# Optimization experiments

Hardware: AMD Instinct MI355X
Metric: run time of the kernel (lower is better)

## Reference

```python
import jax, jax.numpy as jnp
import numpy as np

T, B, P, F = 4096, 64, 512, 5
SHARP = 1.0
NEG_LARGE = -1e30


def setup_inputs() -> dict:
    key = jax.random.key(0)
    k1, k2, k3 = jax.random.split(key, 3)
    x = jax.random.normal(k1, (T, B, F), dtype=jnp.float32)
    # seqs index the 4 base features (feature 4 is the 'stay' score)
    seqs = jax.random.randint(k2, (B, P), 0, 4, dtype=jnp.int32)
    # seqlens index into fwd of width P+1, so valid range is [0, P]
    seqlens = jax.random.randint(k3, (B,), 0, P + 1, dtype=jnp.int32)
    return {"x": x, "seqs": seqs, "seqlens": seqlens}


def reference(x, seqs, seqlens):
    nt, nb, nf = x.shape
    ns = seqs.shape[1]
    # initial forward scores: -inf everywhere except position 0
    fwd0 = jnp.full((nb, ns + 1), NEG_LARGE, dtype=x.dtype).at[:, 0].set(0.0)
    xs = x * SHARP  # [T, B, F]

    def step(fwd, xt):
        # stay: emit the 'stay' feature (index 4), keep position
        stay = xt[:, 4][:, None] + fwd  # [B, P+1]
        # move: emit the base at each sequence position, advance by one
        move = jnp.take_along_axis(xt, seqs, axis=1) + fwd[:, :-1]  # [B, P]
        new = stay.at[:, 1:].set(jnp.logaddexp(move, stay[:, 1:]))
        return new, None

    fwd, _ = jax.lax.scan(step, fwd0, xs)
    # score at final position of each sequence, normalized per time step
    return -jnp.take_along_axis(fwd, seqlens[:, None], axis=1) / (nt * SHARP)
```

## Files before the change

kernel.cpp:

```cpp
#include <hip/hip_runtime.h>
#include <hip/hip_fp16.h>


#define TT 4096
#define BB 64
#define PP 512
#define LN2F 0.69314718055994531f
#define LOG2E 1.44269504088896341f
#define JSTRIDE 1040

typedef unsigned u32x4 __attribute__((ext_vector_type(4)));

__device__ __forceinline__ unsigned f16_bits(float f) {
    return (unsigned)__half_as_ushort(__float2half(f));
}

__global__ __launch_bounds__(256, 1)
void ctc_prepass(const float* __restrict__ x, u32x4* __restrict__ xq) {
    int j = blockIdx.x * 256 + threadIdx.x;
    int b = j >> 12, t = j & 4095;
    const float* r = x + (size_t)(t * 64 + b) * 5;
    float x0 = r[0], x1 = r[1], x2 = r[2], x3 = r[3], x4 = r[4];
    float w0 = fminf(__expf(x0 - x4), 65000.0f);
    float w1 = fminf(__expf(x1 - x4), 65000.0f);
    float w2 = fminf(__expf(x2 - x4), 65000.0f);
    float w3 = fminf(__expf(x3 - x4), 65000.0f);
    u32x4 o;
    o[0] = f16_bits(w0) | (f16_bits(w1) << 16);
    o[1] = f16_bits(w2) | (f16_bits(w3) << 16);
    o[2] = __float_as_uint(x4);
    o[3] = 0u;
    xq[j] = o;
}

__device__ __forceinline__ void gload_lds16(const void* g, void* l) {
    auto gp = (const __attribute__((address_space(1))) void*)(uintptr_t)g;
    auto lp = (__attribute__((address_space(3))) void*)(uintptr_t)l;
    __builtin_amdgcn_global_load_lds(gp, lp, 16, 0, 0);
}

__device__ __forceinline__ int shl1w_i(int s) {
    return __builtin_amdgcn_update_dpp(s, s, 0x138, 0xF, 0xF, false);
}
__device__ __forceinline__ float shl1w_f(float s) {
    return __int_as_float(shl1w_i(__float_as_int(s)));
}
__device__ __forceinline__ int sh1up_i(int s) {
    return __builtin_amdgcn_update_dpp(s, s, 0x130, 0xF, 0xF, false);
}
__device__ __forceinline__ float sh1up_f(float s) {
    return __int_as_float(sh1up_i(__float_as_int(s)));
}

#define FMA_MIX_LO(acc, s, p)                                              \
    asm("v_fma_mix_f32 %0, %1, %2, %0 op_sel:[0,0,0] op_sel_hi:[0,1,0]"    \
        : "+v"(acc) : "v"(s), "v"(p))
#define FMA_MIX_HI(acc, s, p)                                              \
    asm("v_fma_mix_f32 %0, %1, %2, %0 op_sel:[0,1,0] op_sel_hi:[0,1,0]"    \
        : "+v"(acc) : "v"(s), "v"(p))

__global__ __launch_bounds__(64, 1)
void ctc_scan(const u32x4* __restrict__ xq, const int* __restrict__ seqs,
              const int* __restrict__ seqlens, float* __restrict__ jbuf) {
    __shared__ __align__(16) u32x4 ring[512];

    const int b = blockIdx.x >> 1;
    const int w = blockIdx.x & 1;
    const int l = threadIdx.x;
    const bool lane0 = (l == 0);
    const bool lane63 = (l == 63);
    float* const jb = jbuf + (size_t)b * JSTRIDE;

    unsigned ctrl[4];
#pragma unroll
    for (int k = 0; k < 4; ++k) {
        unsigned i0 = (unsigned)seqs[b * PP + 8 * l + 2 * k];
        unsigned i1 = (unsigned)seqs[b * PP + 8 * l + 2 * k + 1];
        ctrl[k] = (2 * i0) | ((2 * i0 + 1) << 8) | ((2 * i1) << 16) | ((2 * i1 + 1) << 24);
    }

    const u32x4* gsrc = xq + (size_t)b * 4096;

    float F[8];
    int M = 0;
    float logs = 0.0f;

    if (w == 0) {
#pragma unroll
        for (int i = 0; i < 8; ++i) F[i] = 0.0f;
#pragma unroll
        for (int c0 = 0; c0 < 4; ++c0)
            gload_lds16(gsrc + c0 * 64 + l, &ring[c0 * 64 + l]);
        asm volatile("s_waitcnt vmcnt(3)" ::: "memory");

        u32x4 wA[8], wB[8];
#pragma unroll
        for (int i = 0; i < 8; ++i) wA[i] = ring[i];
        int nrow = 8;

        auto fwin = [&](u32x4 (&cur)[8], u32x4 (&nxt)[8]) {
            const int rb = nrow & 511;
            nrow += 8;
#pragma unroll
            for (int i = 0; i < 8; ++i) nxt[i] = ring[rb + i];
            asm volatile("" ::: "memory");

            float m = F[0];
#pragma unroll
            for (int i = 1; i < 8; ++i) m = fmaxf(m, F[i]);
            int e2 = ((__float_as_int(m) >> 23) & 0xFF) - 127;
            e2 = (m > 0.0f) ? e2 : 0;
            const int Mp = M + e2;
            const int Mlp = shl1w_i(Mp);
            int dl = (lane0 ? 0 : Mlp) - Mp;
            int dlc = dl > 0 ? dl : 0;
            const int Mnew = Mp + dlc;
            const int sh = Mnew - M;
#pragma unroll
            for (int i = 0; i < 8; ++i) F[i] = ldexpf(F[i], -sh);
            M = Mnew;
            int dn = Mlp - M; dn = dn > 0 ? 0 : dn;
            const float sAx  = lane0 ? 0.0f : ldexpf(1.0f, dn);
            const float cfin = lane0 ? ldexpf(1.0f, -M) : 0.0f;

#pragma unroll
            for (int u = 0; u < 8; ++u) {
                const u32x4 row = cur[u];
                logs += __uint_as_float(row[2]);
                unsigned p0 = __builtin_amdgcn_perm(row[1], row[0], ctrl[0]);
                unsigned p1 = __builtin_amdgcn_perm(row[1], row[0], ctrl[1]);
                unsigned p2 = __builtin_amdgcn_perm(row[1], row[0], ctrl[2]);
                unsigned p3 = __builtin_amdgcn_perm(row[1], row[0], ctrl[3]);
                const float Flr = shl1w_f(F[7]);
                const float fin = fmaf(Flr, sAx, cfin);
                FMA_MIX_HI(F[7], F[6], p3);
                FMA_MIX_LO(F[6], F[5], p3);
                FMA_MIX_HI(F[5], F[4], p2);
                FMA_MIX_LO(F[4], F[3], p2);
                FMA_MIX_HI(F[3], F[2], p1);
                FMA_MIX_LO(F[2], F[1], p1);
                FMA_MIX_HI(F[1], F[0], p0);
                FMA_MIX_LO(F[0], fin,  p0);
            }
        };

#pragma unroll 1
        for (int c = 0; c < 32; ++c) {
            int cs = (c + 4 > 31) ? 31 : (c + 4);
            gload_lds16(gsrc + cs * 64 + l, &ring[((c + 4) & 7) * 64 + l]);
            asm volatile("s_waitcnt vmcnt(3)" ::: "memory");
#pragma unroll 1
            for (int pr = 0; pr < 4; ++pr) { fwin(wA, wB); fwin(wB, wA); }
        }

#pragma unroll
        for (int i = 0; i < 8; ++i) {
            float v = fmaxf(F[i] * 16777216.0f, 1e-38f);
            jb[8 * l + 1 + i] = __log2f(v) - 24.0f + (float)M;
        }
        if (lane0) { jb[0] = 0.0f; jb[1036] = logs * LOG2E; }
    } else {
        const int sl = seqlens[b];
        const bool b512 = (sl == PP);
#pragma unroll
        for (int k = 0; k < 8; ++k) F[k] = (8 * l + k == sl) ? 1.0f : 0.0f;
#pragma unroll
        for (int c0 = 0; c0 < 4; ++c0) {
            const int cp = 63 - c0;
            gload_lds16(gsrc + cp * 64 + l, &ring[(cp & 7) * 64 + l]);
        }
        asm volatile("s_waitcnt vmcnt(3)" ::: "memory");

        u32x4 wA[8], wB[8];
#pragma unroll
        for (int i = 0; i < 8; ++i) wA[i] = ring[511 - i];
        int nbase = 4095 - 8;

        auto bwin = [&](u32x4 (&cur)[8], u32x4 (&nxt)[8]) {
            const int rb = nbase & 511;
            nbase -= 8;
#pragma unroll
            for (int i = 0; i < 8; ++i) nxt[i] = ring[(rb - i) & 511];
            asm volatile("" ::: "memory");

            float m = F[0];
#pragma unroll
            for (int i = 1; i < 8; ++i) m = fmaxf(m, F[i]);
            int e2 = ((__float_as_int(m) >> 23) & 0xFF) - 127;
            e2 = (m > 0.0f) ? e2 : 0;
            const int Mp = M + e2;
            const int Mup = sh1up_i(Mp);
            int nb = lane63 ? (b512 ? 0 : -1048576) : Mup;
            int dl = nb - Mp;
            int dlc = dl > 0 ? dl : 0;
            const int Mnew = Mp + dlc;
            const int sh = Mnew - M;
#pragma unroll
            for (int i = 0; i < 8; ++i) F[i] = ldexpf(F[i], -sh);
            M = Mnew;
            int dn = Mup - M; dn = dn > 0 ? 0 : dn;
            const float sAx  = lane63 ? 0.0f : ldexpf(1.0f, dn);
            const float cfin = (lane63 && b512) ? ldexpf(1.0f, -M) : 0.0f;

#pragma unroll
            for (int u = 0; u < 8; ++u) {
                const u32x4 row = cur[u];
                logs += __uint_as_float(row[2]);
                unsigned p0 = __builtin_amdgcn_perm(row[1], row[0], ctrl[0]);
                unsigned p1 = __builtin_amdgcn_perm(row[1], row[0], ctrl[1]);
                unsigned p2 = __builtin_amdgcn_perm(row[1], row[0], ctrl[2]);
                unsigned p3 = __builtin_amdgcn_perm(row[1], row[0], ctrl[3]);
                const float Bur = sh1up_f(F[0]);
                const float fin = fmaf(Bur, sAx, cfin);
                FMA_MIX_LO(F[0], F[1], p0);
                FMA_MIX_HI(F[1], F[2], p0);
                FMA_MIX_LO(F[2], F[3], p1);
                FMA_MIX_HI(F[3], F[4], p1);
                FMA_MIX_LO(F[4], F[5], p2);
                FMA_MIX_HI(F[5], F[6], p2);
                FMA_MIX_LO(F[6], F[7], p3);
                FMA_MIX_HI(F[7], fin,  p3);
            }
        };

#pragma unroll 1
        for (int c = 0; c < 32; ++c) {
            int cp = 59 - c; cp = cp < 32 ? 32 : cp;
            gload_lds16(gsrc + cp * 64 + l, &ring[(cp & 7) * 64 + l]);
            asm volatile("s_waitcnt vmcnt(3)" ::: "memory");
#pragma unroll 1
            for (int pr = 0; pr < 4; ++pr) { bwin(wA, wB); bwin(wB, wA); }
        }

#pragma unroll
        for (int k = 0; k < 8; ++k) {
            float v = fmaxf(F[k] * 16777216.0f, 1e-38f);
            jb[520 + 8 * l + k] = __log2f(v) - 24.0f + (float)M;
        }
        if (lane0) { jb[520 + PP] = b512 ? 0.0f : -1e30f; jb[1037] = logs * LOG2E; }
    }
}

__global__ __launch_bounds__(64, 1)
void ctc_join(const float* __restrict__ jbuf, float* __restrict__ out) {
    const int b = blockIdx.x;
    const int l = threadIdx.x;
    const float* jb = jbuf + (size_t)b * JSTRIDE;

    float smax = -3.0e38f;
#pragma unroll
    for (int k = 0; k < 9; ++k) {
        const int p = l + (k << 6);
        if (p <= PP) smax = fmaxf(smax, jb[p] + jb[520 + p]);
    }
#pragma unroll
    for (int off = 32; off >= 1; off >>= 1)
        smax = fmaxf(smax, __shfl_xor(smax, off));
    float ssum = 0.0f;
#pragma unroll
    for (int k = 0; k < 9; ++k) {
        const int p = l + (k << 6);
        if (p <= PP) ssum += exp2f((jb[p] + jb[520 + p]) - smax);
    }
#pragma unroll
    for (int off = 32; off >= 1; off >>= 1)
        ssum += __shfl_xor(ssum, off);
    if (l == 0)
        out[b] = -((smax + __log2f(ssum)) + jb[1036] + jb[1037]) * LN2F / (float)TT;
}

extern "C" void kernel_launch(void* const* d_in, const int* in_sizes, int n_in,
                              void* d_out, int out_size, void* d_ws, size_t ws_size,
                              hipStream_t stream) {
    const float* x       = (const float*)d_in[0];
    const int*   seqs    = (const int*)d_in[1];
    const int*   seqlens = (const int*)d_in[2];
    float*       out     = (float*)d_out;
    u32x4*       xq      = (u32x4*)d_ws;
    float*       jbuf    = (float*)((char*)d_ws + (4u << 20));

    ctc_prepass<<<(TT * BB) / 256, 256, 0, stream>>>(x, xq);
    ctc_scan<<<BB * 2, 64, 0, stream>>>(xq, seqs, seqlens, jbuf);
    ctc_join<<<BB, 64, 0, stream>>>(jbuf, out);
}
```

Before: 166.8 us.

## Fuse prepass and join into scan kernel with in-kernel flag handoff

Removes the separate prepass kernel: each scan wave now loads raw x rows directly with per-lane dword loads, computes the exp/fp16 packing itself and writes it to a smaller double-buffered LDS ring. Also removes the join kernel: the forward block stores its results in LDS, spins on a global flag set by the backward block, then performs the log-sum-exp reduction and writes the output. This eliminates two kernel launches and the intermediate xq buffer round trip, at the cost of putting exp work and full load latency (vmcnt(0)) on the serial scan's critical path and relying on co-residency of paired blocks for the spin-wait.

```diff
diff --git a/kernel.cpp b/kernel.cpp
--- a/kernel.cpp
+++ b/kernel.cpp
@@ -7,36 +7,12 @@
 #define PP 512
 #define LN2F 0.69314718055994531f
 #define LOG2E 1.44269504088896341f
-#define JSTRIDE 1040
+#define JSTR 520
 
 typedef unsigned u32x4 __attribute__((ext_vector_type(4)));
 
 __device__ __forceinline__ unsigned f16_bits(float f) {
     return (unsigned)__half_as_ushort(__float2half(f));
-}
-
-__global__ __launch_bounds__(256, 1)
-void ctc_prepass(const float* __restrict__ x, u32x4* __restrict__ xq) {
-    int j = blockIdx.x * 256 + threadIdx.x;
-    int b = j >> 12, t = j & 4095;
-    const float* r = x + (size_t)(t * 64 + b) * 5;
-    float x0 = r[0], x1 = r[1], x2 = r[2], x3 = r[3], x4 = r[4];
-    float w0 = fminf(__expf(x0 - x4), 65000.0f);
-    float w1 = fminf(__expf(x1 - x4), 65000.0f);
-    float w2 = fminf(__expf(x2 - x4), 65000.0f);
-    float w3 = fminf(__expf(x3 - x4), 65000.0f);
-    u32x4 o;
-    o[0] = f16_bits(w0) | (f16_bits(w1) << 16);
-    o[1] = f16_bits(w2) | (f16_bits(w3) << 16);
-    o[2] = __float_as_uint(x4);
-    o[3] = 0u;
-    xq[j] = o;
-}
-
-__device__ __forceinline__ void gload_lds16(const void* g, void* l) {
-    auto gp = (const __attribute__((address_space(1))) void*)(uintptr_t)g;
-    auto lp = (__attribute__((address_space(3))) void*)(uintptr_t)l;
-    __builtin_amdgcn_global_load_lds(gp, lp, 16, 0, 0);
 }
 
 __device__ __forceinline__ int shl1w_i(int s) {
@@ -59,17 +35,43 @@
     asm("v_fma_mix_f32 %0, %1, %2, %0 op_sel:[0,1,0] op_sel_hi:[0,1,0]"    \
         : "+v"(acc) : "v"(s), "v"(p))
 
+#define XLOAD(r0, r1, r2, r3, r4, ptr)                                     \
+    asm volatile(                                                          \
+        "global_load_dword %0, %5, off\n\t"                                \
+        "global_load_dword %1, %5, off offset:4\n\t"                       \
+        "global_load_dword %2, %5, off offset:8\n\t"                       \
+        "global_load_dword %3, %5, off offset:12\n\t"                      \
+        "global_load_dword %4, %5, off offset:16"                          \
+        : "=&v"(r0), "=&v"(r1), "=&v"(r2), "=&v"(r3), "=&v"(r4)            \
+        : "v"(ptr) : "memory")
+
+#define PACK_ROW(par)                                                      \
+    do {                                                                   \
+        float e0 = fminf(__expf(xr0 - xr4), 65000.0f);                     \
+        float e1 = fminf(__expf(xr1 - xr4), 65000.0f);                     \
+        float e2 = fminf(__expf(xr2 - xr4), 65000.0f);                     \
+        float e3 = fminf(__expf(xr3 - xr4), 65000.0f);                     \
+        u32x4 o;                                                           \
+        o[0] = f16_bits(e0) | (f16_bits(e1) << 16);                        \
+        o[1] = f16_bits(e2) | (f16_bits(e3) << 16);                        \
+        o[2] = __float_as_uint(xr4);                                       \
+        o[3] = 0u;                                                         \
+        ring[(par) * 64 + l] = o;                                          \
+    } while (0)
+
 __global__ __launch_bounds__(64, 1)
-void ctc_scan(const u32x4* __restrict__ xq, const int* __restrict__ seqs,
-              const int* __restrict__ seqlens, float* __restrict__ jbuf) {
-    __shared__ __align__(16) u32x4 ring[512];
+void ctc_scan(const float* __restrict__ x, const int* __restrict__ seqs,
+              const int* __restrict__ seqlens, float* __restrict__ jbuf,
+              int* __restrict__ flags, float* __restrict__ out) {
+    __shared__ __align__(16) u32x4 ring[128];
+    __shared__ float gF[PP + 1];
 
     const int b = blockIdx.x >> 1;
     const int w = blockIdx.x & 1;
     const int l = threadIdx.x;
     const bool lane0 = (l == 0);
     const bool lane63 = (l == 63);
-    float* const jb = jbuf + (size_t)b * JSTRIDE;
+    float* const jb = jbuf + (size_t)b * JSTR;
 
     unsigned ctrl[4];
 #pragma unroll
@@ -79,28 +81,33 @@
         ctrl[k] = (2 * i0) | ((2 * i0 + 1) << 8) | ((2 * i1) << 16) | ((2 * i1 + 1) << 24);
     }
 
-    const u32x4* gsrc = xq + (size_t)b * 4096;
+    const float* const xb = x + (size_t)b * 5 + (size_t)l * 320;
 
     float F[8];
     int M = 0;
     float logs = 0.0f;
+    float xr0, xr1, xr2, xr3, xr4;
 
     if (w == 0) {
 #pragma unroll
         for (int i = 0; i < 8; ++i) F[i] = 0.0f;
-#pragma unroll
-        for (int c0 = 0; c0 < 4; ++c0)
-            gload_lds16(gsrc + c0 * 64 + l, &ring[c0 * 64 + l]);
-        asm volatile("s_waitcnt vmcnt(3)" ::: "memory");
+
+        XLOAD(xr0, xr1, xr2, xr3, xr4, xb);
+        asm volatile("s_waitcnt vmcnt(0)" ::: "memory");
+        __builtin_amdgcn_sched_barrier(0);
+        PACK_ROW(0);
+        XLOAD(xr0, xr1, xr2, xr3, xr4, xb + 64 * 320);
+        asm volatile("s_waitcnt lgkmcnt(0)" ::: "memory");
+        __builtin_amdgcn_sched_barrier(0);
 
         u32x4 wA[8], wB[8];
 #pragma unroll
         for (int i = 0; i < 8; ++i) wA[i] = ring[i];
-        int nrow = 8;
+        int nrowF = 8;
 
         auto fwin = [&](u32x4 (&cur)[8], u32x4 (&nxt)[8]) {
-            const int rb = nrow & 511;
-            nrow += 8;
+            const int rb = ((nrowF >> 6) & 1) * 64 + (nrowF & 63);
+            nrowF += 8;
 #pragma unroll
             for (int i = 0; i < 8; ++i) nxt[i] = ring[rb + i];
             asm volatile("" ::: "memory");
@@ -146,9 +153,15 @@
 
 #pragma unroll 1
         for (int c = 0; c < 32; ++c) {
-            int cs = (c + 4 > 31) ? 31 : (c + 4);
-            gload_lds16(gsrc + cs * 64 + l, &ring[((c + 4) & 7) * 64 + l]);
-            asm volatile("s_waitcnt vmcnt(3)" ::: "memory");
+            if (c + 1 < 32) {
+                asm volatile("s_waitcnt vmcnt(0)" ::: "memory");
+                __builtin_amdgcn_sched_barrier(0);
+                PACK_ROW((c + 1) & 1);
+                if (c + 2 < 32)
+                    XLOAD(xr0, xr1, xr2, xr3, xr4, xb + (size_t)(c + 2) * 64 * 320);
+                asm volatile("s_waitcnt lgkmcnt(0)" ::: "memory");
+                __builtin_amdgcn_sched_barrier(0);
+            }
 #pragma unroll 1
             for (int pr = 0; pr < 4; ++pr) { fwin(wA, wB); fwin(wB, wA); }
         }
@@ -156,31 +169,63 @@
 #pragma unroll
         for (int i = 0; i < 8; ++i) {
             float v = fmaxf(F[i] * 16777216.0f, 1e-38f);
-            jb[8 * l + 1 + i] = __log2f(v) - 24.0f + (float)M;
-        }
-        if (lane0) { jb[0] = 0.0f; jb[1036] = logs * LOG2E; }
+            gF[8 * l + 1 + i] = __log2f(v) - 24.0f + (float)M;
+        }
+        if (lane0) gF[0] = 0.0f;
+        asm volatile("s_waitcnt lgkmcnt(0)" ::: "memory");
+        __builtin_amdgcn_sched_barrier(0);
+        const float lgSF = logs * LOG2E;
+
+        if (lane0) {
+            while (__hip_atomic_load(&flags[b], __ATOMIC_ACQUIRE,
+                                     __HIP_MEMORY_SCOPE_AGENT) == 0)
+                __builtin_amdgcn_s_sleep(8);
+        }
+
+        float smax = -3.0e38f;
+#pragma unroll
+        for (int k = 0; k < 9; ++k) {
+            const int p = l + (k << 6);
+            if (p <= PP) smax = fmaxf(smax, gF[p] + jb[p]);
+        }
+#pragma unroll
+        for (int off = 32; off >= 1; off >>= 1)
+            smax = fmaxf(smax, __shfl_xor(smax, off));
+        float ssum = 0.0f;
+#pragma unroll
+        for (int k = 0; k < 9; ++k) {
+            const int p = l + (k << 6);
+            if (p <= PP) ssum += exp2f((gF[p] + jb[p]) - smax);
+        }
+#pragma unroll
+        for (int off = 32; off >= 1; off >>= 1)
+            ssum += __shfl_xor(ssum, off);
+        if (lane0)
+            out[b] = -((smax + __log2f(ssum)) + lgSF + jb[514]) * LN2F / (float)TT;
     } else {
         const int sl = seqlens[b];
         const bool b512 = (sl == PP);
 #pragma unroll
         for (int k = 0; k < 8; ++k) F[k] = (8 * l + k == sl) ? 1.0f : 0.0f;
-#pragma unroll
-        for (int c0 = 0; c0 < 4; ++c0) {
-            const int cp = 63 - c0;
-            gload_lds16(gsrc + cp * 64 + l, &ring[(cp & 7) * 64 + l]);
-        }
-        asm volatile("s_waitcnt vmcnt(3)" ::: "memory");
+
+        XLOAD(xr0, xr1, xr2, xr3, xr4, xb + (size_t)63 * 64 * 320);
+        asm volatile("s_waitcnt vmcnt(0)" ::: "memory");
+        __builtin_amdgcn_sched_barrier(0);
+        PACK_ROW(1);
+        XLOAD(xr0, xr1, xr2, xr3, xr4, xb + (size_t)62 * 64 * 320);
+        asm volatile("s_waitcnt lgkmcnt(0)" ::: "memory");
+        __builtin_amdgcn_sched_barrier(0);
 
         u32x4 wA[8], wB[8];
 #pragma unroll
-        for (int i = 0; i < 8; ++i) wA[i] = ring[511 - i];
-        int nbase = 4095 - 8;
+        for (int i = 0; i < 8; ++i) wA[i] = ring[127 - i];
+        int nbaseB = 4087;
 
         auto bwin = [&](u32x4 (&cur)[8], u32x4 (&nxt)[8]) {
-            const int rb = nbase & 511;
-            nbase -= 8;
-#pragma unroll
-            for (int i = 0; i < 8; ++i) nxt[i] = ring[(rb - i) & 511];
+            const int rb = ((nbaseB >> 6) & 1) * 64 + (nbaseB & 63);
+            nbaseB -= 8;
+#pragma unroll
+            for (int i = 0; i < 8; ++i) nxt[i] = ring[rb - i];
             asm volatile("" ::: "memory");
 
             float m = F[0];
@@ -225,9 +270,15 @@
 
 #pragma unroll 1
         for (int c = 0; c < 32; ++c) {
-            int cp = 59 - c; cp = cp < 32 ? 32 : cp;
-            gload_lds16(gsrc + cp * 64 + l, &ring[(cp & 7) * 64 + l]);
-            asm volatile("s_waitcnt vmcnt(3)" ::: "memory");
+            if (c + 1 < 32) {
+                asm volatile("s_waitcnt vmcnt(0)" ::: "memory");
+                __builtin_amdgcn_sched_barrier(0);
+                PACK_ROW((62 - c) & 1);
+                if (c + 2 < 32)
+                    XLOAD(xr0, xr1, xr2, xr3, xr4, xb + (size_t)(61 - c) * 64 * 320);
+                asm volatile("s_waitcnt lgkmcnt(0)" ::: "memory");
+                __builtin_amdgcn_sched_barrier(0);
+            }
 #pragma unroll 1
             for (int pr = 0; pr < 4; ++pr) { bwin(wA, wB); bwin(wB, wA); }
         }
@@ -235,38 +286,14 @@
 #pragma unroll
         for (int k = 0; k < 8; ++k) {
             float v = fmaxf(F[k] * 16777216.0f, 1e-38f);
-            jb[520 + 8 * l + k] = __log2f(v) - 24.0f + (float)M;
-        }
-        if (lane0) { jb[520 + PP] = b512 ? 0.0f : -1e30f; jb[1037] = logs * LOG2E; }
+            jb[8 * l + k] = __log2f(v) - 24.0f + (float)M;
+        }
+        if (lane0) { jb[512] = b512 ? 0.0f : -1e30f; jb[514] = logs * LOG2E; }
+        __threadfence();
+        if (lane0)
+            __hip_atomic_store(&flags[b], 1, __ATOMIC_RELEASE,
+                               __HIP_MEMORY_SCOPE_AGENT);
     }
-}
-
-__global__ __launch_bounds__(64, 1)
-void ctc_join(const float* __restrict__ jbuf, float* __restrict__ out) {
-    const int b = blockIdx.x;
-    const int l = threadIdx.x;
-    const float* jb = jbuf + (size_t)b * JSTRIDE;
-
-    float smax = -3.0e38f;
-#pragma unroll
-    for (int k = 0; k < 9; ++k) {
-        const int p = l + (k << 6);
-        if (p <= PP) smax = fmaxf(smax, jb[p] + jb[520 + p]);
-    }
-#pragma unroll
-    for (int off = 32; off >= 1; off >>= 1)
-        smax = fmaxf(smax, __shfl_xor(smax, off));
-    float ssum = 0.0f;
-#pragma unroll
-    for (int k = 0; k < 9; ++k) {
-        const int p = l + (k << 6);
-        if (p <= PP) ssum += exp2f((jb[p] + jb[520 + p]) - smax);
-    }
-#pragma unroll
-    for (int off = 32; off >= 1; off >>= 1)
-        ssum += __shfl_xor(ssum, off);
-    if (l == 0)
-        out[b] = -((smax + __log2f(ssum)) + jb[1036] + jb[1037]) * LN2F / (float)TT;
 }
 
 extern "C" void kernel_launch(void* const* d_in, const int* in_sizes, int n_in,
@@ -276,10 +303,9 @@
     const int*   seqs    = (const int*)d_in[1];
     const int*   seqlens = (const int*)d_in[2];
     float*       out     = (float*)d_out;
-    u32x4*       xq      = (u32x4*)d_ws;
-    float*       jbuf    = (float*)((char*)d_ws + (4u << 20));
-
-    ctc_prepass<<<(TT * BB) / 256, 256, 0, stream>>>(x, xq);
-    ctc_scan<<<BB * 2, 64, 0, stream>>>(xq, seqs, seqlens, jbuf);
-    ctc_join<<<BB, 64, 0, stream>>>(jbuf, out);
-}
+    float*       jbuf    = (float*)d_ws;
+    int*         flags   = (int*)((char*)d_ws + BB * JSTR * 4);
+
+    hipMemsetAsync(flags, 0, BB * sizeof(int), stream);
+    ctc_scan<<<BB * 2, 64, 0, stream>>>(x, seqs, seqlens, jbuf, flags, out);
+}
```

Result: no change. 166.4 us (-0.3%).
